# Performance work log

Hardware: AMD Instinct MI355X
Metric: run time of the kernel (lower is better)

The kernel has to match this reference:

```python
import jax, jax.numpy as jnp
import numpy as np

B, E, C = 128, 16, 128   # batch, n experts (program tokens), module_dim
H = W = 64               # input image size
PROJ, FC, NANS = 512, 1024, 2


def conv2d(x, w, b, padding=1):
    # x: [N,C,H,W], w: [O,I,kh,kw]
    y = jax.lax.conv_general_dilated(
        x, w, (1, 1), [(padding, padding), (padding, padding)],
        dimension_numbers=('NCHW', 'OIHW', 'NCHW'))
    return y + b[None, :, None, None]


def maxpool2(x):
    return jax.lax.reduce_window(x, -jnp.inf, jax.lax.max, (1, 1, 2, 2), (1, 1, 2, 2), 'VALID')


def setup_inputs() -> dict:
    key = jax.random.key(0)
    ks = jax.random.split(key, 12)
    def init(k, shape, fan_in):
        return jax.random.normal(k, shape, jnp.float32) * np.float32(1.0 / np.sqrt(fan_in))
    inp = {}
    inp['image'] = jax.random.normal(ks[0], (B, 3, H, W), jnp.float32)
    inp['question'] = jax.random.randint(ks[1], (B, 8), 0, E)
    # stem: conv3x3 3->C, relu, maxpool2, conv3x3 C->C, relu, maxpool2
    inp['stem_w1'] = init(ks[2], (C, 3, 3, 3), 3 * 9)
    inp['stem_b1'] = jnp.zeros((C,), jnp.float32)
    inp['stem_w2'] = init(ks[3], (C, C, 3, 3), C * 9)
    inp['stem_b2'] = jnp.zeros((C,), jnp.float32)
    # E expert residual blocks, each: conv3x3 C->C, relu, conv3x3 C->C, +res, relu
    inp['exp_w1'] = init(ks[4], (E, C, C, 3, 3), C * 9)
    inp['exp_b1'] = jnp.zeros((E, C), jnp.float32)
    inp['exp_w2'] = init(ks[5], (E, C, C, 3, 3), C * 9)
    inp['exp_b2'] = jnp.zeros((E, C), jnp.float32)
    # classifier: 1x1 conv C->PROJ, relu, maxpool2, flatten, fc->FC, relu, fc->NANS
    inp['proj_w'] = init(ks[6], (PROJ, C, 1, 1), C)
    inp['proj_b'] = jnp.zeros((PROJ,), jnp.float32)
    inp['fc1_w'] = init(ks[7], (FC, PROJ * 8 * 8), PROJ * 8 * 8)
    inp['fc1_b'] = jnp.zeros((FC,), jnp.float32)
    inp['fc2_w'] = init(ks[8], (NANS, FC), FC)
    inp['fc2_b'] = jnp.zeros((NANS,), jnp.float32)
    return inp


def reference(image, question, stem_w1, stem_b1, stem_w2, stem_b2,
              exp_w1, exp_b1, exp_w2, exp_b2,
              proj_w, proj_b, fc1_w, fc1_b, fc2_w, fc2_b):
    # stem -> [B, C, 16, 16]
    h = maxpool2(jax.nn.relu(conv2d(image, stem_w1, stem_b1)))
    h = maxpool2(jax.nn.relu(conv2d(h, stem_w2, stem_b2)))

    def block(x, w1, b1, w2, b2):
        # per-sample residual block with per-sample expert weights; x: [C,h,w]
        x4 = x[None]
        out = jax.nn.relu(conv2d(x4, w1, b1))
        out = conv2d(out, w2, b2)
        return jax.nn.relu(x4 + out)[0]

    # dispatch order matches [color_lhs, lhs, color_rhs, rhs, rel] = cols 3,4,6,7,5
    for col in (3, 4, 6, 7, 5):
        idx = question[:, col]
        h = jax.vmap(block)(h, exp_w1[idx], exp_b1[idx], exp_w2[idx], exp_b2[idx])

    # classifier
    p = maxpool2(jax.nn.relu(conv2d(h, proj_w, proj_b, padding=0)))  # [B,PROJ,8,8]
    f = p.reshape(p.shape[0], -1)
    f = jax.nn.relu(f @ fc1_w.T + fc1_b)
    return f @ fc2_w.T + fc2_b
```

## Files before the change

### kernel.cpp

```cpp
#include <hip/hip_runtime.h>
#include <hip/hip_bf16.h>
#include <cstdint>
#include <cstddef>


typedef __bf16 bf16_t;
typedef __attribute__((ext_vector_type(4))) bf16_t bf16x4;
typedef __attribute__((ext_vector_type(8))) bf16_t bf16x8;
typedef __attribute__((ext_vector_type(16))) float f32x16;
typedef __attribute__((ext_vector_type(4))) float f32x4;

__global__ __launch_bounds__(256) void prep_stem1_k(
    const float* __restrict__ exp_w1, const float* __restrict__ exp_w2,
    const float* __restrict__ stem_w2, const float* __restrict__ proj_w,
    bf16_t* __restrict__ wT1, bf16_t* __restrict__ wT2,
    bf16_t* __restrict__ wTs2, bf16_t* __restrict__ pwT,
    const float* __restrict__ img, const float* __restrict__ w1,
    const float* __restrict__ b1, bf16_t* __restrict__ s1out)
{
  alignas(16) __shared__ char smem[37120];
  int bid = blockIdx.x;
  const int tid = threadIdx.x;

  if (bid >= 328) {
    bid -= 328;
    float* sImg = (float*)smem;
    char*  sOut = smem + 4112;
    const int b = bid >> 4, t = bid & 15;
    const int ty0p = (t >> 2) * 8, tx0p = (t & 3) * 8;
    const int lane = tid & 63;
    const int wvbase = __builtin_amdgcn_readfirstlane(tid >> 6) * 32;

    for (int s = tid; s < 972; s += 256) {
      const int ic = s / 324, r2 = s - ic * 324;
      const int rr = r2 / 18, cc = r2 - rr * 18;
      const int gy = 2 * ty0p - 1 + rr, gx = 2 * tx0p - 1 + cc;
      float v = 0.f;
      if (gy >= 0 && gy < 64 && gx >= 0 && gx < 64)
        v = img[(((size_t)b * 3 + ic) * 64 + gy) * 64 + gx];
      sImg[ic * 342 + rr * 19 + cc] = v;
    }
    __syncthreads();

    const int ppy = lane >> 3, ppx = lane & 7;
    const int swz = (lane & 15) << 3;
    char* orow = sOut + lane * 256;

    for (int oc8 = 0; oc8 < 32; oc8 += 8) {
      float acc[8][2][2];
#pragma unroll
      for (int q = 0; q < 8; ++q) {
        const float bv = b1[wvbase + oc8 + q];
#pragma unroll
        for (int i = 0; i < 2; ++i)
#pragma unroll
          for (int jj = 0; jj < 2; ++jj) acc[q][i][jj] = bv;
      }
#pragma unroll
      for (int ic = 0; ic < 3; ++ic)
#pragma unroll
        for (int dy = 0; dy < 3; ++dy)
#pragma unroll
          for (int dx = 0; dx < 3; ++dx) {
            const float p00 = sImg[ic * 342 + (2 * ppy + dy) * 19 + 2 * ppx + dx];
            const float p01 = sImg[ic * 342 + (2 * ppy + dy) * 19 + 2 * ppx + dx + 1];
            const float p10 = sImg[ic * 342 + (2 * ppy + dy + 1) * 19 + 2 * ppx + dx];
            const float p11 = sImg[ic * 342 + (2 * ppy + dy + 1) * 19 + 2 * ppx + dx + 1];
#pragma unroll
            for (int q = 0; q < 8; ++q) {
              const float wv2 = w1[(wvbase + oc8 + q) * 27 + ic * 9 + dy * 3 + dx];
              acc[q][0][0] = fmaf(p00, wv2, acc[q][0][0]);
              acc[q][0][1] = fmaf(p01, wv2, acc[q][0][1]);
              acc[q][1][0] = fmaf(p10, wv2, acc[q][1][0]);
              acc[q][1][1] = fmaf(p11, wv2, acc[q][1][1]);
            }
          }
#pragma unroll
      for (int h4 = 0; h4 < 8; h4 += 4) {
        bf16x4 qv;
#pragma unroll
        for (int j = 0; j < 4; ++j) {
          const int q = h4 + j;
          const float mx = fmaxf(fmaxf(acc[q][0][0], acc[q][0][1]),
                                 fmaxf(acc[q][1][0], acc[q][1][1]));
          qv[j] = (bf16_t)fmaxf(mx, 0.f);
        }
        *(bf16x4*)(orow + (((wvbase + oc8 + h4) * 2) ^ swz)) = qv;
      }
    }
    __syncthreads();

#pragma unroll
    for (int it = 0; it < 4; ++it) {
      const int idx = it * 256 + tid;
      const int px = idx >> 4, ch8 = idx & 15;
      const int sw = (px & 15) << 3;
      const char* rb = sOut + px * 256;
      bf16x4 lo = *(const bf16x4*)(rb + ((ch8 * 16) ^ sw));
      bf16x4 hi = *(const bf16x4*)(rb + ((ch8 * 16 + 8) ^ sw));
      bf16x8 v;
#pragma unroll
      for (int j = 0; j < 4; ++j) { v[j] = lo[j]; v[4 + j] = hi[j]; }
      const int gpy = ty0p + (px >> 3), gpx = tx0p + (px & 7);
      *(bf16x8*)(s1out + ((size_t)(b * 1024 + gpy * 32 + gpx)) * 128 + ch8 * 8) = v;
    }
    return;
  }

  if (bid >= 264) {
    const int base = (bid - 264) * 1024 + tid;
#pragma unroll
    for (int it = 0; it < 4; ++it) {
      const int idx = base + it * 256;
      const int oc = idx >> 7, ic = idx & 127;
      const int og = oc >> 5, cc2 = oc & 31;
      const int ich2 = ic >> 6, icl = ic & 63;
      const int kh2 = icl >> 4, g2 = (icl >> 3) & 1, j2 = icl & 7;
      const int off = ((((og * 2 + ich2) * 4 + kh2) << 9)) + ((g2 << 5) + cc2) * 8 + j2;
      pwT[off] = (bf16_t)proj_w[(size_t)oc * 128 + ic];
    }
    return;
  }

  const float* in;
  bf16_t* out;
  if (bid < 128)      { in = exp_w1;  out = wT1; }
  else if (bid < 256) { in = exp_w2;  out = wT2;  bid -= 128; }
  else                { in = stem_w2; out = wTs2; bid -= 256; }
  const int e   = bid >> 3;
  const int rem = bid & 7;
  const int ocg = rem >> 1, ich = rem & 1;

  float* sW = (float*)smem;
  bf16_t* outb = out + (size_t)e * 147456;

  for (int h = 0; h < 2; ++h) {
    if (h) __syncthreads();
    for (int idx = tid; idx < 2304; idx += 256) {
      const int r16 = idx / 144, q = idx - r16 * 144;
      const float* src = in + (size_t)(e * 128 + ocg * 32 + h * 16 + r16) * 1152
                       + ich * 576 + q * 4;
      *(f32x4*)(&sW[r16 * 580 + q * 4]) = *(const f32x4*)src;
    }
    __syncthreads();
    for (int c = tid; c < 1152; c += 256) {
      const int dd  = c >> 7;
      const int kh  = (c >> 5) & 3;
      const int g2  = (c >> 4) & 1;
      const int c16 = c & 15;
      const int cc  = h * 16 + c16;
      bf16x8 v;
#pragma unroll
      for (int j = 0; j < 8; ++j)
        v[j] = (bf16_t)sW[c16 * 580 + (kh * 16 + g2 * 8 + j) * 9 + dd];
      bf16_t* op = outb + ((size_t)(((ocg * 2 + ich) * 9 + dd) * 4 + kh) << 9)
                 + (g2 * 32 + cc) * 8;
      *(bf16x8*)op = v;
    }
  }
}

__global__ __launch_bounds__(256) void conv_stem2_k(
    const bf16_t* __restrict__ act, const bf16_t* __restrict__ wF,
    const float* __restrict__ bias, bf16_t* __restrict__ out)
{
  const int b = blockIdx.x >> 4, ph = blockIdx.x & 15;
  const int y0 = ph * 2;
  const int tid = threadIdx.x, lane = tid & 63, wv = tid >> 6;
  const int g = lane >> 5, cc = lane & 31;
  const int wq = wv;

  __shared__ bf16_t simg[272 * 64];

  f32x16 acc[2];
#pragma unroll
  for (int i = 0; i < 2; ++i)
#pragma unroll
    for (int r = 0; r < 16; ++r) acc[i][r] = 0.f;

  const bf16_t* wfb = wF + ((size_t)(wq * 2) * 9 * 4 << 9) + lane * 8;

  for (int p = tid; p < 272; p += 256) {
    const int ich = p / 136, r2 = p - ich * 136;
    const int yy = r2 / 34, xx = r2 - yy * 34;
    const int gy = y0 + yy - 1, gx = xx - 1;
    const bool inb = (gy >= 0 && gy < 32 && gx >= 0 && gx < 32);
    const bf16_t* src = act + ((size_t)(b * 1024 + gy * 32 + gx)) * 128 + ich * 64;
#pragma unroll
    for (int j = 0; j < 8; ++j) {
      bf16x8 v = {};
      if (inb) v = *(const bf16x8*)(src + j * 8);
      const int waddr = (p * 128 + j * 16) ^ ((p & 7) << 4);
      *(bf16x8*)((char*)simg + waddr) = v;
    }
  }
  __syncthreads();

#pragma unroll
  for (int ich = 0; ich < 2; ++ich) {
#pragma unroll
    for (int dydx = 0; dydx < 9; ++dydx) {
      const int dy = dydx / 3, dx = dydx - dy * 3;
      const bf16_t* wf = wfb + (((ich * 9 + dydx) * 4) << 9);
#pragma unroll
      for (int kh = 0; kh < 4; ++kh) {
        const bf16x8 a = *(const bf16x8*)(wf + (kh << 9));
#pragma unroll
        for (int r = 0; r < 2; ++r) {
          const int s = ich * 136 + (r + dy) * 34 + cc + dx;
          const int raddr = (s * 128 + (kh * 2 + g) * 16) ^ ((s & 7) << 4);
          const bf16x8 bbv = *(const bf16x8*)((const char*)simg + raddr);
          acc[r] = __builtin_amdgcn_mfma_f32_32x32x16_bf16(a, bbv, acc[r], 0, 0, 0);
        }
      }
    }
  }

  const int pxp = cc >> 1;
  bf16_t* op = out + ((size_t)(b * 256 + ph * 16 + pxp)) * 128;
#pragma unroll
  for (int rq = 0; rq < 4; ++rq) {
    const int oc4 = wq * 32 + rq * 8 + g * 4;
    const f32x4 bi = *(const f32x4*)(bias + oc4);
    bf16x4 qv;
#pragma unroll
    for (int j = 0; j < 4; ++j) {
      const int r = rq * 4 + j;
      float v = fmaxf(acc[0][r], acc[1][r]);
      v = fmaxf(v, __shfl_xor(v, 1));
      qv[j] = (bf16_t)fmaxf(v + bi[j], 0.f);
    }
    if ((cc & 1) == 0) *(bf16x4*)(op + oc4) = qv;
  }
}

template<int RES>
__global__ __launch_bounds__(256) void conv_exp_k(
    const bf16_t* __restrict__ act, const bf16_t* __restrict__ wF,
    const float* __restrict__ bias, const int* __restrict__ question, int col,
    const bf16_t* __restrict__ res, bf16_t* __restrict__ out)
{
  const int b = blockIdx.x >> 2, ph = blockIdx.x & 3;
  const int y0 = ph * 4;
  const int e = question[b * 8 + col];
  const int tid = threadIdx.x, lane = tid & 63, wv = tid >> 6;
  const int g = lane >> 5, cc = lane & 31;
  const int wq_oc = wv & 1, wq_px = wv >> 1;

  __shared__ bf16_t simg[216 * 64];

  f32x16 acc[2];
#pragma unroll
  for (int i = 0; i < 2; ++i)
#pragma unroll
    for (int r = 0; r < 16; ++r) acc[i][r] = 0.f;

  const int px = wq_px * 32 + cc;
  const int sl = (px >> 4) * 18 + (px & 15);

  const bf16_t* wfb = wF + (size_t)e * 147456
                    + (((size_t)(wq_oc * 2) * 2) * 9 * 4 << 9) + lane * 8;

  for (int p = tid; p < 216; p += 256) {
    const int ich = p / 108, r2 = p - ich * 108;
    const int yy = r2 / 18, xx = r2 - yy * 18;
    const int gy = y0 + yy - 1, gx = xx - 1;
    const bool inb = (gy >= 0 && gy < 16 && gx >= 0 && gx < 16);
    const bf16_t* src = act + ((size_t)(b * 256 + gy * 16 + gx)) * 128 + ich * 64;
#pragma unroll
    for (int j = 0; j < 8; ++j) {
      bf16x8 v = {};
      if (inb) v = *(const bf16x8*)(src + j * 8);
      const int waddr = (p * 128 + j * 16) ^ ((p & 7) << 4);
      *(bf16x8*)((char*)simg + waddr) = v;
    }
  }
  __syncthreads();

#pragma unroll
  for (int ich = 0; ich < 2; ++ich) {
#pragma unroll
    for (int dydx = 0; dydx < 9; ++dydx) {
      const int dy = dydx / 3, dx = dydx - dy * 3;
      const int sbase = ich * 108 + sl + dy * 18 + dx;
      const bf16_t* wf = wfb + (((ich * 9 + dydx) * 4) << 9);
#pragma unroll
      for (int kh = 0; kh < 4; ++kh) {
        const bf16x8 a0 = *(const bf16x8*)(wf + (kh << 9));
        const bf16x8 a1 = *(const bf16x8*)(wf + 36864 + (kh << 9));
        const int raddr = (sbase * 128 + (kh * 2 + g) * 16) ^ ((sbase & 7) << 4);
        const bf16x8 bbv = *(const bf16x8*)((const char*)simg + raddr);
        acc[0] = __builtin_amdgcn_mfma_f32_32x32x16_bf16(a0, bbv, acc[0], 0, 0, 0);
        acc[1] = __builtin_amdgcn_mfma_f32_32x32x16_bf16(a1, bbv, acc[1], 0, 0, 0);
      }
    }
  }

  const float* bb = bias + e * 128;
  const size_t pixbase = ((size_t)(b * 256 + (y0 + (px >> 4)) * 16 + (px & 15))) * 128;
  bf16_t* op = out + pixbase;
#pragma unroll
  for (int mf = 0; mf < 2; ++mf) {
#pragma unroll
    for (int rq = 0; rq < 4; ++rq) {
      const int oc4 = wq_oc * 64 + mf * 32 + rq * 8 + g * 4;
      const f32x4 bi = *(const f32x4*)(bb + oc4);
      bf16x4 qv;
      bf16x4 rv = {};
      if (RES) rv = *(const bf16x4*)(res + pixbase + oc4);
#pragma unroll
      for (int j = 0; j < 4; ++j) {
        float v = acc[mf][rq * 4 + j] + bi[j];
        if (RES) v += (float)rv[j];
        qv[j] = (bf16_t)fmaxf(v, 0.f);
      }
      *(bf16x4*)(op + oc4) = qv;
    }
  }
}

__global__ __launch_bounds__(256) void proj_mfma_k(
    const bf16_t* __restrict__ h, const bf16_t* __restrict__ pwF,
    const float* __restrict__ pb, bf16_t* __restrict__ f)
{
  const int b = blockIdx.x >> 2, ocg = blockIdx.x & 3;
  const int tid = threadIdx.x, lane = tid & 63, wv = tid >> 6;
  const int g = lane >> 5, cc = lane & 31;
  const int wq_oc = wv & 1, wq_px = wv >> 1;

  __shared__ bf16_t simg[256 * 64];

  f32x16 acc[2][4];
#pragma unroll
  for (int i = 0; i < 2; ++i)
#pragma unroll
    for (int j = 0; j < 4; ++j)
#pragma unroll
      for (int r = 0; r < 16; ++r) acc[i][j][r] = 0.f;

  const int px0 = wq_px * 128 + cc;
  const int og0 = ocg * 4 + wq_oc * 2;
  const bf16_t* pfb = pwF + (((size_t)og0 * 2 * 4) << 9) + lane * 8;

  for (int ich = 0; ich < 2; ++ich) {
    __syncthreads();
    {
      const int p = tid;
      const bf16_t* src = h + ((size_t)(b * 256 + p)) * 128 + ich * 64;
#pragma unroll
      for (int j = 0; j < 8; ++j) {
        bf16x8 v = *(const bf16x8*)(src + j * 8);
        const int waddr = (p * 128 + j * 16) ^ ((p & 7) << 4);
        *(bf16x8*)((char*)simg + waddr) = v;
      }
    }
    __syncthreads();

#pragma unroll
    for (int kh = 0; kh < 4; ++kh) {
      const bf16x8 a0 = *(const bf16x8*)(pfb + ((ich * 4 + kh) << 9));
      const bf16x8 a1 = *(const bf16x8*)(pfb + 4096 + ((ich * 4 + kh) << 9));
#pragma unroll
      for (int nf = 0; nf < 4; ++nf) {
        const int s = px0 + nf * 32;
        const int raddr = (s * 128 + (kh * 2 + g) * 16) ^ ((s & 7) << 4);
        const bf16x8 bb = *(const bf16x8*)((const char*)simg + raddr);
        acc[0][nf] = __builtin_amdgcn_mfma_f32_32x32x16_bf16(a0, bb, acc[0][nf], 0, 0, 0);
        acc[1][nf] = __builtin_amdgcn_mfma_f32_32x32x16_bf16(a1, bb, acc[1][nf], 0, 0, 0);
      }
    }
  }

#pragma unroll
  for (int mf = 0; mf < 2; ++mf) {
#pragma unroll
    for (int nf = 0; nf < 4; ++nf) {
      const int px = px0 + nf * 32;
      const int x = px & 15;
      const int py = wq_px * 4 + nf;
      const int pxp = x >> 1;
#pragma unroll
      for (int r = 0; r < 16; ++r) {
        float v = acc[mf][nf][r];
        v = fmaxf(v, __shfl_xor(v, 1));
        v = fmaxf(v, __shfl_xor(v, 16));
        const int oc = ocg * 128 + wq_oc * 64 + mf * 32 + (r & 3) + 8 * (r >> 2) + 4 * g;
        v = fmaxf(v + pb[oc], 0.f);
        if ((cc & 17) == 0)
          f[((size_t)(b * 512 + oc)) * 64 + py * 8 + pxp] = (bf16_t)v;
      }
    }
  }
}

__global__ __launch_bounds__(256) void fc1_mfma_k(
    const bf16_t* __restrict__ A, const float* __restrict__ W,
    float* __restrict__ part)
{
  const int nt = blockIdx.x;
  const int ks = blockIdx.y;
  const int n0 = nt * 64;
  const int k0 = ks * 1024;
  const int tid = threadIdx.x, lane = tid & 63, wv = tid >> 6;
  const int g = lane >> 5, cc = lane & 31;
  const int mh = wv & 1, nh = wv >> 1;

  __shared__ char sA[16384];
  __shared__ char sB[8192];

  f32x16 acc0, acc1;
#pragma unroll
  for (int r = 0; r < 16; ++r) { acc0[r] = 0.f; acc1[r] = 0.f; }

  for (int t = 0; t < 16; ++t) {
    __syncthreads();
#pragma unroll
    for (int i = 0; i < 4; ++i) {
      const int c = tid + i * 256;
      const int row = c >> 3, ko = c & 7;
      bf16x8 v = *(const bf16x8*)(A + (size_t)row * 32768 + k0 + t * 64 + ko * 8);
      const int wa = (row * 128 + ko * 16) ^ ((row & 7) << 4);
      *(bf16x8*)(sA + wa) = v;
    }
#pragma unroll
    for (int i = 0; i < 2; ++i) {
      const int c = tid + i * 256;
      const int row = c >> 3, ko = c & 7;
      const float* src = W + (size_t)(n0 + row) * 32768 + k0 + t * 64 + ko * 8;
      f32x4 u0 = *(const f32x4*)src;
      f32x4 u1 = *(const f32x4*)(src + 4);
      bf16x8 v;
#pragma unroll
      for (int j = 0; j < 4; ++j) { v[j] = (bf16_t)u0[j]; v[4 + j] = (bf16_t)u1[j]; }
      const int wa = (row * 128 + ko * 16) ^ ((row & 7) << 4);
      *(bf16x8*)(sB + wa) = v;
    }
    __syncthreads();
#pragma unroll
    for (int kss = 0; kss < 4; ++kss) {
      const int kb = kss * 32 + g * 16;
      const int rA0 = mh * 64 + cc, rA1 = rA0 + 32;
      const bf16x8 a0 = *(const bf16x8*)(sA + ((rA0 * 128 + kb) ^ ((rA0 & 7) << 4)));
      const bf16x8 a1 = *(const bf16x8*)(sA + ((rA1 * 128 + kb) ^ ((rA1 & 7) << 4)));
      const int rB = nh * 32 + cc;
      const bf16x8 bb = *(const bf16x8*)(sB + ((rB * 128 + kb) ^ ((rB & 7) << 4)));
      acc0 = __builtin_amdgcn_mfma_f32_32x32x16_bf16(a0, bb, acc0, 0, 0, 0);
      acc1 = __builtin_amdgcn_mfma_f32_32x32x16_bf16(a1, bb, acc1, 0, 0, 0);
    }
  }

  float* pp = part + ((size_t)ks * 128) * 1024 + n0 + nh * 32 + cc;
#pragma unroll
  for (int r = 0; r < 16; ++r) {
    const int m0 = mh * 64 + (r & 3) + 8 * (r >> 2) + 4 * g;
    pp[(size_t)m0 * 1024] = acc0[r];
    pp[(size_t)(m0 + 32) * 1024] = acc1[r];
  }
}

__global__ __launch_bounds__(256) void fc1_red_k(
    const float* __restrict__ part, const float* __restrict__ bias, float* __restrict__ fo)
{
  const int i = blockIdx.x * 256 + threadIdx.x;
  const int m = i >> 10, j = i & 1023;
  float s = bias[j];
#pragma unroll
  for (int ks = 0; ks < 32; ++ks) s += part[((size_t)ks * 128 + m) * 1024 + j];
  fo[i] = fmaxf(s, 0.f);
}

__global__ __launch_bounds__(256) void fc2_k(
    const float* __restrict__ fo, const float* __restrict__ w2,
    const float* __restrict__ b2, float* __restrict__ out)
{
  const int m = blockIdx.x;
  const int tid = threadIdx.x;
  float a0 = 0.f, a1 = 0.f;
  for (int k = tid; k < 1024; k += 256) {
    const float fv = fo[(size_t)m * 1024 + k];
    a0 = fmaf(fv, w2[k], a0);
    a1 = fmaf(fv, w2[1024 + k], a1);
  }
#pragma unroll
  for (int o = 32; o > 0; o >>= 1) {
    a0 += __shfl_down(a0, o);
    a1 += __shfl_down(a1, o);
  }
  __shared__ float r0[4], r1[4];
  const int wid = tid >> 6;
  if ((tid & 63) == 0) { r0[wid] = a0; r1[wid] = a1; }
  __syncthreads();
  if (tid == 0) {
    out[(size_t)m * 2 + 0] = r0[0] + r0[1] + r0[2] + r0[3] + b2[0];
    out[(size_t)m * 2 + 1] = r1[0] + r1[1] + r1[2] + r1[3] + b2[1];
  }
}

extern "C" void kernel_launch(void* const* d_in, const int* in_sizes, int n_in,
                              void* d_out, int out_size, void* d_ws, size_t ws_size,
                              hipStream_t stream)
{
  const float* image    = (const float*)d_in[0];
  const int*   question = (const int*)  d_in[1];
  const float* stem_w1  = (const float*)d_in[2];
  const float* stem_b1  = (const float*)d_in[3];
  const float* stem_w2  = (const float*)d_in[4];
  const float* stem_b2  = (const float*)d_in[5];
  const float* exp_w1   = (const float*)d_in[6];
  const float* exp_b1   = (const float*)d_in[7];
  const float* exp_w2   = (const float*)d_in[8];
  const float* exp_b2   = (const float*)d_in[9];
  const float* proj_w   = (const float*)d_in[10];
  const float* proj_b   = (const float*)d_in[11];
  const float* fc1_w    = (const float*)d_in[12];
  const float* fc1_b    = (const float*)d_in[13];
  const float* fc2_w    = (const float*)d_in[14];
  const float* fc2_b    = (const float*)d_in[15];
  float* out = (float*)d_out;

  char* base = (char*)d_ws;
  bf16_t* actA   = (bf16_t*)(base + 33554432);
  bf16_t* actH   = (bf16_t*)(base + 67108864);
  bf16_t* actT   = (bf16_t*)(base + 75497472);
  bf16_t* wT1    = (bf16_t*)(base + 83886080);
  bf16_t* wT2    = (bf16_t*)(base + 88604672);
  bf16_t* wTs2   = (bf16_t*)(base + 93323264);
  bf16_t* pwT    = (bf16_t*)(base + 93618176);
  bf16_t* fbf  = (bf16_t*)base;
  float*  part = (float*)(base + 8388608);
  float*  f1o  = (float*)(base + 25165824);

  prep_stem1_k<<<2376, 256, 0, stream>>>(exp_w1, exp_w2, stem_w2, proj_w,
                                         wT1, wT2, wTs2, pwT,
                                         image, stem_w1, stem_b1, actA);

  conv_stem2_k<<<2048, 256, 0, stream>>>(actA, wTs2, stem_b2, actH);

  const int cols[5] = {3, 4, 6, 7, 5};
  for (int i = 0; i < 5; ++i) {
    conv_exp_k<0><<<512, 256, 0, stream>>>(actH, wT1, exp_b1, question, cols[i],
                                           nullptr, actT);
    conv_exp_k<1><<<512, 256, 0, stream>>>(actT, wT2, exp_b2, question, cols[i],
                                           actH, actH);
  }

  proj_mfma_k<<<512, 256, 0, stream>>>(actH, pwT, proj_b, fbf);
  fc1_mfma_k<<<dim3(16, 32), 256, 0, stream>>>(fbf, fc1_w, part);
  fc1_red_k<<<512, 256, 0, stream>>>(part, fc1_b, f1o);
  fc2_k<<<128, 256, 0, stream>>>(f1o, fc2_w, fc2_b, out);
}
```

Baseline: 354.9 us.

## Compute stem conv1 with bf16 MFMA via im2col tiles instead of scalar FMA

Rewrites the first stem 3x3 conv (3->128 channels) branch to build an im2col tile in shared memory and run 32x32x16 bf16 MFMA instructions, with the 2x2 maxpool done by lane shuffles. Each block now covers a smaller 4x16 pixel tile, so the grid grows to 8520 blocks. This replaces scalar fp32 FMA work and the staged output transpose, at the cost of bf16 rounding of image and weights before accumulation and more blocks with redundant weight loads. Bias is now added after the max rather than before it, which is equivalent.

```diff
diff --git a/kernel.cpp b/kernel.cpp
--- a/kernel.cpp
+++ b/kernel.cpp
@@ -24,85 +24,93 @@
 
   if (bid >= 328) {
     bid -= 328;
-    float* sImg = (float*)smem;
-    char*  sOut = smem + 4112;
-    const int b = bid >> 4, t = bid & 15;
-    const int ty0p = (t >> 2) * 8, tx0p = (t & 3) * 8;
-    const int lane = tid & 63;
-    const int wvbase = __builtin_amdgcn_readfirstlane(tid >> 6) * 32;
-
-    for (int s = tid; s < 972; s += 256) {
-      const int ic = s / 324, r2 = s - ic * 324;
-      const int rr = r2 / 18, cc = r2 - rr * 18;
-      const int gy = 2 * ty0p - 1 + rr, gx = 2 * tx0p - 1 + cc;
+    const int b  = bid >> 6;
+    const int t  = bid & 63;
+    const int ty = t >> 2, tx = t & 3;
+    const int y0 = ty * 4, x0 = tx * 16;
+    const int lane = tid & 63, wv = tid >> 6;
+    const int g = lane >> 5, p = lane & 31;
+
+    float*  sImg = (float*)smem;
+    bf16_t* sCol = (bf16_t*)(smem + 1296);
+
+    for (int s2 = tid; s2 < 324; s2 += 256) {
+      const int ic = s2 / 108, r2 = s2 - ic * 108;
+      const int rr = r2 / 18, cc2 = r2 - rr * 18;
+      const int gy = y0 - 1 + rr, gx = x0 - 1 + cc2;
       float v = 0.f;
       if (gy >= 0 && gy < 64 && gx >= 0 && gx < 64)
         v = img[(((size_t)b * 3 + ic) * 64 + gy) * 64 + gx];
-      sImg[ic * 342 + rr * 19 + cc] = v;
-    }
-    __syncthreads();
-
-    const int ppy = lane >> 3, ppx = lane & 7;
-    const int swz = (lane & 15) << 3;
-    char* orow = sOut + lane * 256;
-
-    for (int oc8 = 0; oc8 < 32; oc8 += 8) {
-      float acc[8][2][2];
-#pragma unroll
-      for (int q = 0; q < 8; ++q) {
-        const float bv = b1[wvbase + oc8 + q];
-#pragma unroll
-        for (int i = 0; i < 2; ++i)
-#pragma unroll
-          for (int jj = 0; jj < 2; ++jj) acc[q][i][jj] = bv;
-      }
-#pragma unroll
-      for (int ic = 0; ic < 3; ++ic)
-#pragma unroll
-        for (int dy = 0; dy < 3; ++dy)
-#pragma unroll
-          for (int dx = 0; dx < 3; ++dx) {
-            const float p00 = sImg[ic * 342 + (2 * ppy + dy) * 19 + 2 * ppx + dx];
-            const float p01 = sImg[ic * 342 + (2 * ppy + dy) * 19 + 2 * ppx + dx + 1];
-            const float p10 = sImg[ic * 342 + (2 * ppy + dy + 1) * 19 + 2 * ppx + dx];
-            const float p11 = sImg[ic * 342 + (2 * ppy + dy + 1) * 19 + 2 * ppx + dx + 1];
-#pragma unroll
-            for (int q = 0; q < 8; ++q) {
-              const float wv2 = w1[(wvbase + oc8 + q) * 27 + ic * 9 + dy * 3 + dx];
-              acc[q][0][0] = fmaf(p00, wv2, acc[q][0][0]);
-              acc[q][0][1] = fmaf(p01, wv2, acc[q][0][1]);
-              acc[q][1][0] = fmaf(p10, wv2, acc[q][1][0]);
-              acc[q][1][1] = fmaf(p11, wv2, acc[q][1][1]);
-            }
-          }
-#pragma unroll
-      for (int h4 = 0; h4 < 8; h4 += 4) {
+      sImg[ic * 108 + rr * 18 + cc2] = v;
+    }
+
+    bf16x8 a0[2], a1[2];
+#pragma unroll
+    for (int ogi = 0; ogi < 2; ++ogi) {
+      const int og = (wv & 1) * 2 + ogi;
+      const float* wrow = w1 + (size_t)(og * 32 + p) * 27;
+#pragma unroll
+      for (int j = 0; j < 8; ++j) {
+        a0[ogi][j] = (bf16_t)wrow[g * 8 + j];
+        const int k1 = 16 + g * 8 + j;
+        a1[ogi][j] = (k1 < 27) ? (bf16_t)wrow[k1] : (bf16_t)0.f;
+      }
+    }
+    __syncthreads();
+
+    {
+      const int k = tid & 31;
+      const int tpb = tid >> 5;
+      const bool kv = k < 27;
+      const int ic = k / 9, rem = k - ic * 9;
+      const int dy = rem / 3, dx = rem - dy * 3;
+#pragma unroll
+      for (int i = 0; i < 8; ++i) {
+        const int tp = tpb + i * 8;
+        const int py = tp >> 4, px = tp & 15;
+        const float v = kv ? sImg[ic * 108 + (py + dy) * 18 + px + dx] : 0.f;
+        sCol[tp * 32 + k] = (bf16_t)v;
+      }
+    }
+    __syncthreads();
+
+    const int tp = (wv >> 1) * 32 + p;
+    const bf16x8 bfr0 = *(const bf16x8*)(sCol + tp * 32 + g * 8);
+    const bf16x8 bfr1 = *(const bf16x8*)(sCol + tp * 32 + 16 + g * 8);
+
+    f32x16 acc[2];
+#pragma unroll
+    for (int i = 0; i < 2; ++i)
+#pragma unroll
+      for (int r = 0; r < 16; ++r) acc[i][r] = 0.f;
+
+#pragma unroll
+    for (int ogi = 0; ogi < 2; ++ogi) {
+      acc[ogi] = __builtin_amdgcn_mfma_f32_32x32x16_bf16(a0[ogi], bfr0, acc[ogi], 0, 0, 0);
+      acc[ogi] = __builtin_amdgcn_mfma_f32_32x32x16_bf16(a1[ogi], bfr1, acc[ogi], 0, 0, 0);
+    }
+
+    const int gpy = ty * 2 + (wv >> 1);
+    const int gpx = tx * 8 + (p >> 1);
+    const bool wr = (p & 17) == 0;
+    bf16_t* op = s1out + ((size_t)(b * 1024 + gpy * 32 + gpx)) * 128;
+#pragma unroll
+    for (int ogi = 0; ogi < 2; ++ogi) {
+      const int og = (wv & 1) * 2 + ogi;
+#pragma unroll
+      for (int rq = 0; rq < 4; ++rq) {
+        const int oc4 = og * 32 + rq * 8 + g * 4;
+        const f32x4 bi = *(const f32x4*)(b1 + oc4);
         bf16x4 qv;
 #pragma unroll
         for (int j = 0; j < 4; ++j) {
-          const int q = h4 + j;
-          const float mx = fmaxf(fmaxf(acc[q][0][0], acc[q][0][1]),
-                                 fmaxf(acc[q][1][0], acc[q][1][1]));
-          qv[j] = (bf16_t)fmaxf(mx, 0.f);
+          float v = acc[ogi][rq * 4 + j];
+          v = fmaxf(v, __shfl_xor(v, 1));
+          v = fmaxf(v, __shfl_xor(v, 16));
+          qv[j] = (bf16_t)fmaxf(v + bi[j], 0.f);
         }
-        *(bf16x4*)(orow + (((wvbase + oc8 + h4) * 2) ^ swz)) = qv;
-      }
-    }
-    __syncthreads();
-
-#pragma unroll
-    for (int it = 0; it < 4; ++it) {
-      const int idx = it * 256 + tid;
-      const int px = idx >> 4, ch8 = idx & 15;
-      const int sw = (px & 15) << 3;
-      const char* rb = sOut + px * 256;
-      bf16x4 lo = *(const bf16x4*)(rb + ((ch8 * 16) ^ sw));
-      bf16x4 hi = *(const bf16x4*)(rb + ((ch8 * 16 + 8) ^ sw));
-      bf16x8 v;
-#pragma unroll
-      for (int j = 0; j < 4; ++j) { v[j] = lo[j]; v[4 + j] = hi[j]; }
-      const int gpy = ty0p + (px >> 3), gpx = tx0p + (px & 7);
-      *(bf16x8*)(s1out + ((size_t)(b * 1024 + gpy * 32 + gpx)) * 128 + ch8 * 8) = v;
+        if (wr) *(bf16x4*)(op + oc4) = qv;
+      }
     }
     return;
   }
@@ -530,7 +538,7 @@
   float*  part = (float*)(base + 8388608);
   float*  f1o  = (float*)(base + 25165824);
 
-  prep_stem1_k<<<2376, 256, 0, stream>>>(exp_w1, exp_w2, stem_w2, proj_w,
+  prep_stem1_k<<<8520, 256, 0, stream>>>(exp_w1, exp_w2, stem_w2, proj_w,
                                          wT1, wT2, wTs2, pwT,
                                          image, stem_w1, stem_b1, actA);
 
```

New measurement: 365.4 us. 1.03x slower.
